# Kernel optimization log

Hardware: AMD Instinct MI355X
Metric: run time of the kernel (lower is better)

## Reference

```python
import jax, jax.numpy as jnp
import numpy as np


def setup_inputs() -> dict:
    key = jax.random.key(0)
    k1, k2, k3, k4 = jax.random.split(key, 4)
    B, C, H, W = 8, 256, 64, 64
    x = jax.random.normal(k1, (B, C, H, W), dtype=jnp.float32)
    wq = jax.random.normal(k2, (1, C), dtype=jnp.float32) * (1.0 / np.sqrt(C))
    wk = jax.random.normal(k3, (1, C), dtype=jnp.float32) * (1.0 / np.sqrt(C))
    wv = jax.random.normal(k4, (C, C), dtype=jnp.float32) * (1.0 / np.sqrt(C))
    gamma = jnp.zeros((1,), dtype=jnp.float32)
    return {"x": x, "wq": wq, "wk": wk, "wv": wv, "gamma": gamma}


def reference(x, wq, wk, wv, gamma):
    B, C, H, W = x.shape
    N = H * W
    xf = x.reshape(B, C, N)                      # [B, C, N]
    # 1x1 convs == channel matmuls
    f = jnp.einsum('oc,bcn->bon', wq, xf)        # [B, 1, N]
    g = jnp.einsum('oc,bcn->bon', wk, xf)        # [B, 1, N]
    h = jnp.einsum('oc,bcn->bon', wv, xf)        # [B, C, N]
    # scores[b, i, j] = f[b, 0, i] * g[b, 0, j]  -> [B, N, N]
    scores = jnp.einsum('bi,bj->bij', f[:, 0, :], g[:, 0, :])
    # softmax over dim=1 (rows), matching torch F.softmax(..., dim=1)
    beta = jax.nn.softmax(scores, axis=1)        # [B, N, N]
    gam = gamma[0]
    o = (1.0 - gam) * jnp.einsum('bcn,bnm->bcm', h, beta) + gam * xf
    return o.reshape(B, C, H, W)
```

## Files before the change

kernel.cpp:

```cpp
#include <hip/hip_runtime.h>
#include <math.h>

#define BQ 8
#define CQ 256
#define NQ 4096
#define MT 128
#define NSUP 64

typedef short s16x8 __attribute__((ext_vector_type(8)));
typedef short s16x4 __attribute__((ext_vector_type(4)));
typedef float f32x4 __attribute__((ext_vector_type(4)));
typedef unsigned int uint;

static __device__ __forceinline__ float4 ld4(const float* p) { return *(const float4*)p; }

static constexpr float LOG2E = 1.4426950408889634f;

static __device__ __forceinline__ short f2bf(float f) {
    return __builtin_bit_cast(short, (__bf16)f);
}
static __device__ __forceinline__ uint fkey(float f) {
    uint b = __builtin_bit_cast(uint, f);
    return b ^ (0x80000000u | (uint)((int)b >> 31));
}
static __device__ __forceinline__ float fdec(uint u) {
    uint b = (u & 0x80000000u) ? (u ^ 0x80000000u) : ~u;
    return __builtin_bit_cast(float, b);
}

__global__ void k_fg(const float* __restrict__ x, const float* __restrict__ wq,
                     const float* __restrict__ wk, float* __restrict__ fs,
                     float* __restrict__ g, short* __restrict__ xbf,
                     uint* __restrict__ fmxu, uint* __restrict__ fmnu) {
    int b = blockIdx.y;
    int t = threadIdx.x;
    int nl = (t & 31) * 2;
    int cg = t >> 5;
    int n = blockIdx.x * 64 + nl;
    const float* xb = x + (size_t)b * CQ * NQ + n;
    uint* xo = (uint*)(xbf + (size_t)b * CQ * NQ + n);
    float f0 = 0.f, f1 = 0.f, g0 = 0.f, g1 = 0.f;
    int c0 = cg * 32;
#pragma unroll 8
    for (int c = c0; c < c0 + 32; ++c) {
        float2 v = *(const float2*)&xb[(size_t)c * NQ];
        f0 = fmaf(wq[c], v.x, f0);
        f1 = fmaf(wq[c], v.y, f1);
        g0 = fmaf(wk[c], v.x, g0);
        g1 = fmaf(wk[c], v.y, g1);
        uint p = (uint)(unsigned short)f2bf(v.x) | ((uint)(unsigned short)f2bf(v.y) << 16);
        xo[c * (NQ / 2)] = p;
    }
    __shared__ float sf[8][64], sg2[8][64];
    sf[cg][nl] = f0;  sf[cg][nl + 1] = f1;
    sg2[cg][nl] = g0; sg2[cg][nl + 1] = g1;
    __syncthreads();
    if (t < 64) {
        float f = 0.f, gg = 0.f;
#pragma unroll
        for (int i = 0; i < 8; ++i) { f += sf[i][t]; gg += sg2[i][t]; }
        f *= LOG2E;
        fs[b * NQ + blockIdx.x * 64 + t] = f;
        g[b * NQ + blockIdx.x * 64 + t]  = gg;
        float mx = f, mn = f;
#pragma unroll
        for (int off = 32; off; off >>= 1) {
            mx = fmaxf(mx, __shfl_xor(mx, off));
            mn = fminf(mn, __shfl_xor(mn, off));
        }
        if (t == 0) {
            atomicMax(&fmxu[b], fkey(mx));
            atomicMin(&fmnu[b], fkey(mn));
        }
    }
}

#define FLDS_OFF 131072
#define ZBUF_OFF 147456
#define SMEM_BYTES 149504

#define STAGE_PAIR(bufp, pi)                                                       \
    {                                                                              \
        int cpair2_ = (pi) * 2;                                                    \
        _Pragma("unroll")                                                          \
        for (int r2_ = 0; r2_ < 4; ++r2_) {                                        \
            int off_ = tid * 16 + r2_ * 8192;                                      \
            int half_ = off_ >> 14;                                                \
            int rem_ = off_ & 16383;                                               \
            int row_ = rem_ >> 6;                                                  \
            int lq_ = ((rem_ >> 4) & 3) ^ ((row_ >> 1) & 3);                       \
            const short* src_ = xb + (size_t)row_ * NQ + (cpair2_ + half_) * 32 + lq_ * 8; \
            __builtin_amdgcn_global_load_lds(                                      \
                (const __attribute__((address_space(1))) void*)src_,               \
                (__attribute__((address_space(3))) void*)((bufp) + off_), 16, 0, 0); \
        }                                                                          \
    }

__global__ void __launch_bounds__(512, 1) k_attn(
    const short* __restrict__ xbf, const float* __restrict__ fsp,
    const float* __restrict__ gp, const uint* __restrict__ fmxu,
    const uint* __restrict__ fmnu, const float* __restrict__ wv,
    const float* __restrict__ x, const float* __restrict__ gamma,
    float* __restrict__ out) {
    __shared__ __align__(16) char smem[SMEM_BYTES];

    int bid = blockIdx.x;
    int b = bid & 7;
    int mblk = bid >> 3;
    int m0 = mblk * MT;
    int tid = threadIdx.x;
    int l = tid & 63;
    int w = tid >> 6;
    int ws = w & 1;
    int wm = (w >> 1) & 1;
    int wc = w >> 2;
    int q = l >> 4;
    int cr = l & 15;
    int qp16 = (q ^ ((cr >> 1) & 3)) * 16;

    const short* xb = xbf + (size_t)b * CQ * NQ;
    const float* fb = fsp + b * NQ;

#pragma unroll
    for (int r2 = 0; r2 < 2; ++r2) {
        int off = tid * 16 + r2 * 8192;
        __builtin_amdgcn_global_load_lds(
            (const __attribute__((address_space(1))) void*)(fb + (off >> 2)),
            (__attribute__((address_space(3))) void*)(smem + FLDS_OFF + off), 16, 0, 0);
    }
    STAGE_PAIR(smem, 0)

    float fmx = fdec(fmxu[b]), fmn = fdec(fmnu[b]);
    const float* gb = gp + b * NQ;
    float gj[4], nM[4], zac[4];
#pragma unroll
    for (int jm = 0; jm < 4; ++jm) {
        float gv = gb[m0 + wm * 64 + jm * 16 + cr];
        gj[jm] = gv;
        nM[jm] = -((gv >= 0.f) ? gv * fmx : gv * fmn);
        zac[jm] = 0.f;
    }

    f32x4 acc[8][4];
#pragma unroll
    for (int jc = 0; jc < 8; ++jc)
#pragma unroll
        for (int jm = 0; jm < 4; ++jm) acc[jc][jm] = (f32x4){0.f, 0.f, 0.f, 0.f};

    __syncthreads();

    for (int s = 0; s < NSUP; ++s) {
        char* nbuf = smem + ((s & 1) ^ 1) * 32768;
        if (s < NSUP - 1) STAGE_PAIR(nbuf, s + 1)

        int chunk = 2 * s + ws;
        const char* cbuf = smem + (s & 1) * 32768 + ws * 16384;
        const float* fls = (const float*)(smem + FLDS_OFF) + chunk * 32;
        float4 fqa = *(const float4*)(fls + q * 8);
        float4 fqb = *(const float4*)(fls + q * 8 + 4);
        float fq[8] = {fqa.x, fqa.y, fqa.z, fqa.w, fqb.x, fqb.y, fqb.z, fqb.w};
        s16x8 bv[4];
#pragma unroll
        for (int jm = 0; jm < 4; ++jm) {
            float z = zac[jm];
#pragma unroll
            for (int i = 0; i < 8; ++i) {
                float e = __builtin_amdgcn_exp2f(fmaf(fq[i], gj[jm], nM[jm]));
                z += e;
                bv[jm][i] = f2bf(e);
            }
            zac[jm] = z;
        }
#pragma unroll
        for (int jc = 0; jc < 8; ++jc) {
            s16x8 av = *(const s16x8*)(cbuf + (wc * 128 + jc * 16 + cr) * 64 + qp16);
#pragma unroll
            for (int jm = 0; jm < 4; ++jm)
                acc[jc][jm] = __builtin_amdgcn_mfma_f32_16x16x32_bf16(av, bv[jm], acc[jc][jm], 0, 0, 0);
        }
        __syncthreads();
    }

    float zf[4];
#pragma unroll
    for (int jm = 0; jm < 4; ++jm) {
        float z = zac[jm];
        z += __shfl_xor(z, 16);
        z += __shfl_xor(z, 32);
        zf[jm] = z;
    }
    float* zb = (float*)(smem + ZBUF_OFF);
    if (q == 0) {
#pragma unroll
        for (int jm = 0; jm < 4; ++jm) zb[w * 64 + jm * 16 + cr] = zf[jm];
    }
    __syncthreads();
#pragma unroll
    for (int jm = 0; jm < 4; ++jm) zf[jm] += zb[(w ^ 1) * 64 + jm * 16 + cr];

    {
        int p = wc * 2 + wm;
        float* mrg = (float*)(smem + p * 32768);
        if (ws == 1) {
#pragma unroll
            for (int jc = 0; jc < 8; ++jc)
#pragma unroll
                for (int jm = 0; jm < 4; ++jm)
                    *(f32x4*)(mrg + ((jc * 4 + jm) * 64 + l) * 4) = acc[jc][jm];
        }
        __syncthreads();
        if (ws == 0) {
#pragma unroll
            for (int jc = 0; jc < 8; ++jc)
#pragma unroll
                for (int jm = 0; jm < 4; ++jm) {
                    f32x4 o = *(const f32x4*)(mrg + ((jc * 4 + jm) * 64 + l) * 4);
                    acc[jc][jm] += o;
                }
        }
        __syncthreads();
    }

    if (ws == 0) {
        float rzl[4];
#pragma unroll
        for (int jm = 0; jm < 4; ++jm) rzl[jm] = 1.0f / zf[jm];
#pragma unroll
        for (int jc = 0; jc < 8; ++jc) {
#pragma unroll
            for (int jm = 0; jm < 4; ++jm) {
                int mloc = wm * 64 + jm * 16 + cr;
                int cb = (wc * 256 + jc * 32 + q * 8) ^ ((mloc & 7) << 4);
                s16x4 v;
#pragma unroll
                for (int r = 0; r < 4; ++r) v[r] = f2bf(acc[jc][jm][r] * rzl[jm]);
                *(s16x4*)(smem + mloc * 512 + cb) = v;
            }
        }
    }
    __syncthreads();

    int co0 = w * 32;
    f32x4 acc2[2][8];
#pragma unroll
    for (int j2 = 0; j2 < 2; ++j2)
#pragma unroll
        for (int jm2 = 0; jm2 < 8; ++jm2) acc2[j2][jm2] = (f32x4){0.f, 0.f, 0.f, 0.f};

#pragma unroll 2
    for (int ks = 0; ks < 8; ++ks) {
        s16x8 a2[2];
#pragma unroll
        for (int j2 = 0; j2 < 2; ++j2) {
            const float* wr = wv + (size_t)(co0 + j2 * 16 + cr) * CQ + ks * 32 + q * 8;
            float4 wa = ld4(wr);
            float4 wb = ld4(wr + 4);
            a2[j2][0] = f2bf(wa.x); a2[j2][1] = f2bf(wa.y);
            a2[j2][2] = f2bf(wa.z); a2[j2][3] = f2bf(wa.w);
            a2[j2][4] = f2bf(wb.x); a2[j2][5] = f2bf(wb.y);
            a2[j2][6] = f2bf(wb.z); a2[j2][7] = f2bf(wb.w);
        }
#pragma unroll
        for (int jm2 = 0; jm2 < 8; ++jm2) {
            int mloc = jm2 * 16 + cr;
            s16x8 b2 = *(const s16x8*)(smem + mloc * 512 + ((ks * 64 + q * 16) ^ ((mloc & 7) << 4)));
#pragma unroll
            for (int j2 = 0; j2 < 2; ++j2)
                acc2[j2][jm2] = __builtin_amdgcn_mfma_f32_16x16x32_bf16(a2[j2], b2, acc2[j2][jm2], 0, 0, 0);
        }
    }

    float gam = gamma[0];
    float omg = 1.f - gam;
    if (gam != 0.f) {
#pragma unroll
        for (int j2 = 0; j2 < 2; ++j2)
#pragma unroll
            for (int jm2 = 0; jm2 < 8; ++jm2)
#pragma unroll
                for (int r = 0; r < 4; ++r) {
                    int c_out = co0 + j2 * 16 + q * 4 + r;
                    size_t idx = ((size_t)b * CQ + c_out) * NQ + m0 + jm2 * 16 + cr;
                    __builtin_nontemporal_store(
                        fmaf(gam, x[idx], acc2[j2][jm2][r] * omg), out + idx);
                }
    } else {
#pragma unroll
        for (int j2 = 0; j2 < 2; ++j2)
#pragma unroll
            for (int jm2 = 0; jm2 < 8; ++jm2)
#pragma unroll
                for (int r = 0; r < 4; ++r) {
                    int c_out = co0 + j2 * 16 + q * 4 + r;
                    size_t idx = ((size_t)b * CQ + c_out) * NQ + m0 + jm2 * 16 + cr;
                    __builtin_nontemporal_store(acc2[j2][jm2][r] * omg, out + idx);
                }
    }
}

extern "C" void kernel_launch(void* const* d_in, const int* in_sizes, int n_in,
                              void* d_out, int out_size, void* d_ws, size_t ws_size,
                              hipStream_t stream) {
    const float* x     = (const float*)d_in[0];
    const float* wq    = (const float*)d_in[1];
    const float* wk    = (const float*)d_in[2];
    const float* wv    = (const float*)d_in[3];
    const float* gamma = (const float*)d_in[4];
    float* out = (float*)d_out;

    float* ws  = (float*)d_ws;
    float* fs  = ws;
    float* g   = ws + BQ * NQ;
    uint* fmxu = (uint*)(ws + 2 * BQ * NQ);
    uint* fmnu = fmxu + 8;
    short* xbf = (short*)(ws + 2 * BQ * NQ + 64);

    hipMemsetAsync(fmxu, 0x00, 32, stream);
    hipMemsetAsync(fmnu, 0xFF, 32, stream);
    hipLaunchKernelGGL(k_fg, dim3(NQ / 64, BQ), dim3(256), 0, stream,
                       x, wq, wk, fs, g, xbf, fmxu, fmnu);
    hipLaunchKernelGGL(k_attn, dim3(BQ * (NQ / MT)), dim3(512), 0, stream,
                       xbf, fs, g, fmxu, fmnu, wv, x, gamma, out);
}
```

Baseline: 119.8 us.

## Double attention block to 1024 threads, halving per-wave tiles and staging work

Doubles the attention kernel block from 512 to 1024 threads (16 waves). Each wave now owns 32 instead of 64 output columns in the score/value MFMA phase and 16 instead of 32 output channels in the projection phase, which halves accumulator registers and adds more waves for latency hiding. The staging macro is replaced by precomputed per-thread source/destination pointers, so each thread issues two LDS-direct loads per step. The trade-off is more waves sharing the same LDS buffers and barriers, repeated exp work per wave for the same columns, and the __launch_bounds__(1024,4) hint combined with ~146KB of LDS per block.

```diff
diff --git a/kernel.cpp b/kernel.cpp
--- a/kernel.cpp
+++ b/kernel.cpp
@@ -79,24 +79,7 @@
 #define ZBUF_OFF 147456
 #define SMEM_BYTES 149504
 
-#define STAGE_PAIR(bufp, pi)                                                       \
-    {                                                                              \
-        int cpair2_ = (pi) * 2;                                                    \
-        _Pragma("unroll")                                                          \
-        for (int r2_ = 0; r2_ < 4; ++r2_) {                                        \
-            int off_ = tid * 16 + r2_ * 8192;                                      \
-            int half_ = off_ >> 14;                                                \
-            int rem_ = off_ & 16383;                                               \
-            int row_ = rem_ >> 6;                                                  \
-            int lq_ = ((rem_ >> 4) & 3) ^ ((row_ >> 1) & 3);                       \
-            const short* src_ = xb + (size_t)row_ * NQ + (cpair2_ + half_) * 32 + lq_ * 8; \
-            __builtin_amdgcn_global_load_lds(                                      \
-                (const __attribute__((address_space(1))) void*)src_,               \
-                (__attribute__((address_space(3))) void*)((bufp) + off_), 16, 0, 0); \
-        }                                                                          \
-    }
-
-__global__ void __launch_bounds__(512, 1) k_attn(
+__global__ void __launch_bounds__(1024, 4) k_attn(
     const short* __restrict__ xbf, const float* __restrict__ fsp,
     const float* __restrict__ gp, const uint* __restrict__ fmxu,
     const uint* __restrict__ fmnu, const float* __restrict__ wv,
@@ -112,8 +95,8 @@
     int l = tid & 63;
     int w = tid >> 6;
     int ws = w & 1;
-    int wm = (w >> 1) & 1;
-    int wc = w >> 2;
+    int wm = (w >> 1) & 3;
+    int wc = w >> 3;
     int q = l >> 4;
     int cr = l & 15;
     int qp16 = (q ^ ((cr >> 1) & 3)) * 16;
@@ -121,47 +104,65 @@
     const short* xb = xbf + (size_t)b * CQ * NQ;
     const float* fb = fsp + b * NQ;
 
-#pragma unroll
-    for (int r2 = 0; r2 < 2; ++r2) {
-        int off = tid * 16 + r2 * 8192;
-        __builtin_amdgcn_global_load_lds(
-            (const __attribute__((address_space(1))) void*)(fb + (off >> 2)),
-            (__attribute__((address_space(3))) void*)(smem + FLDS_OFF + off), 16, 0, 0);
-    }
-    STAGE_PAIR(smem, 0)
+    int dst0 = tid * 16;
+    int dst1 = tid * 16 + 16384;
+    int srow = tid >> 2;
+    int slq = (tid & 3) ^ ((srow >> 1) & 3);
+    const short* src0 = xb + (size_t)srow * NQ + slq * 8;
+    const short* src1 = src0 + 32;
+
+    __builtin_amdgcn_global_load_lds(
+        (const __attribute__((address_space(1))) void*)(fb + tid * 4),
+        (__attribute__((address_space(3))) void*)(smem + FLDS_OFF + tid * 16), 16, 0, 0);
+    __builtin_amdgcn_global_load_lds(
+        (const __attribute__((address_space(1))) void*)src0,
+        (__attribute__((address_space(3))) void*)(smem + dst0), 16, 0, 0);
+    __builtin_amdgcn_global_load_lds(
+        (const __attribute__((address_space(1))) void*)src1,
+        (__attribute__((address_space(3))) void*)(smem + dst1), 16, 0, 0);
+    src0 += 64;
+    src1 += 64;
 
     float fmx = fdec(fmxu[b]), fmn = fdec(fmnu[b]);
     const float* gb = gp + b * NQ;
-    float gj[4], nM[4], zac[4];
-#pragma unroll
-    for (int jm = 0; jm < 4; ++jm) {
-        float gv = gb[m0 + wm * 64 + jm * 16 + cr];
+    float gj[2], nM[2], zac[2];
+#pragma unroll
+    for (int jm = 0; jm < 2; ++jm) {
+        float gv = gb[m0 + wm * 32 + jm * 16 + cr];
         gj[jm] = gv;
         nM[jm] = -((gv >= 0.f) ? gv * fmx : gv * fmn);
         zac[jm] = 0.f;
     }
 
-    f32x4 acc[8][4];
+    f32x4 acc[8][2];
 #pragma unroll
     for (int jc = 0; jc < 8; ++jc)
 #pragma unroll
-        for (int jm = 0; jm < 4; ++jm) acc[jc][jm] = (f32x4){0.f, 0.f, 0.f, 0.f};
+        for (int jm = 0; jm < 2; ++jm) acc[jc][jm] = (f32x4){0.f, 0.f, 0.f, 0.f};
 
     __syncthreads();
 
     for (int s = 0; s < NSUP; ++s) {
-        char* nbuf = smem + ((s & 1) ^ 1) * 32768;
-        if (s < NSUP - 1) STAGE_PAIR(nbuf, s + 1)
-
+        if (s < NSUP - 1) {
+            char* nbuf = smem + ((s + 1) & 1) * 32768;
+            __builtin_amdgcn_global_load_lds(
+                (const __attribute__((address_space(1))) void*)src0,
+                (__attribute__((address_space(3))) void*)(nbuf + dst0), 16, 0, 0);
+            __builtin_amdgcn_global_load_lds(
+                (const __attribute__((address_space(1))) void*)src1,
+                (__attribute__((address_space(3))) void*)(nbuf + dst1), 16, 0, 0);
+            src0 += 64;
+            src1 += 64;
+        }
         int chunk = 2 * s + ws;
         const char* cbuf = smem + (s & 1) * 32768 + ws * 16384;
         const float* fls = (const float*)(smem + FLDS_OFF) + chunk * 32;
         float4 fqa = *(const float4*)(fls + q * 8);
         float4 fqb = *(const float4*)(fls + q * 8 + 4);
         float fq[8] = {fqa.x, fqa.y, fqa.z, fqa.w, fqb.x, fqb.y, fqb.z, fqb.w};
-        s16x8 bv[4];
-#pragma unroll
-        for (int jm = 0; jm < 4; ++jm) {
+        s16x8 bv[2];
+#pragma unroll
+        for (int jm = 0; jm < 2; ++jm) {
             float z = zac[jm];
 #pragma unroll
             for (int i = 0; i < 8; ++i) {
@@ -174,16 +175,15 @@
 #pragma unroll
         for (int jc = 0; jc < 8; ++jc) {
             s16x8 av = *(const s16x8*)(cbuf + (wc * 128 + jc * 16 + cr) * 64 + qp16);
-#pragma unroll
-            for (int jm = 0; jm < 4; ++jm)
-                acc[jc][jm] = __builtin_amdgcn_mfma_f32_16x16x32_bf16(av, bv[jm], acc[jc][jm], 0, 0, 0);
+            acc[jc][0] = __builtin_amdgcn_mfma_f32_16x16x32_bf16(av, bv[0], acc[jc][0], 0, 0, 0);
+            acc[jc][1] = __builtin_amdgcn_mfma_f32_16x16x32_bf16(av, bv[1], acc[jc][1], 0, 0, 0);
         }
         __syncthreads();
     }
 
-    float zf[4];
-#pragma unroll
-    for (int jm = 0; jm < 4; ++jm) {
+    float zf[2];
+#pragma unroll
+    for (int jm = 0; jm < 2; ++jm) {
         float z = zac[jm];
         z += __shfl_xor(z, 16);
         z += __shfl_xor(z, 32);
@@ -192,29 +192,29 @@
     float* zb = (float*)(smem + ZBUF_OFF);
     if (q == 0) {
 #pragma unroll
-        for (int jm = 0; jm < 4; ++jm) zb[w * 64 + jm * 16 + cr] = zf[jm];
+        for (int jm = 0; jm < 2; ++jm) zb[w * 32 + jm * 16 + cr] = zf[jm];
     }
     __syncthreads();
 #pragma unroll
-    for (int jm = 0; jm < 4; ++jm) zf[jm] += zb[(w ^ 1) * 64 + jm * 16 + cr];
+    for (int jm = 0; jm < 2; ++jm) zf[jm] += zb[(w ^ 1) * 32 + jm * 16 + cr];
 
     {
-        int p = wc * 2 + wm;
-        float* mrg = (float*)(smem + p * 32768);
+        int p = wc * 4 + wm;
+        float* mrg = (float*)(smem + p * 16384);
         if (ws == 1) {
 #pragma unroll
             for (int jc = 0; jc < 8; ++jc)
 #pragma unroll
-                for (int jm = 0; jm < 4; ++jm)
-                    *(f32x4*)(mrg + ((jc * 4 + jm) * 64 + l) * 4) = acc[jc][jm];
+                for (int jm = 0; jm < 2; ++jm)
+                    *(f32x4*)(mrg + ((jc * 2 + jm) * 64 + l) * 4) = acc[jc][jm];
         }
         __syncthreads();
         if (ws == 0) {
 #pragma unroll
             for (int jc = 0; jc < 8; ++jc)
 #pragma unroll
-                for (int jm = 0; jm < 4; ++jm) {
-                    f32x4 o = *(const f32x4*)(mrg + ((jc * 4 + jm) * 64 + l) * 4);
+                for (int jm = 0; jm < 2; ++jm) {
+                    f32x4 o = *(const f32x4*)(mrg + ((jc * 2 + jm) * 64 + l) * 4);
                     acc[jc][jm] += o;
                 }
         }
@@ -222,14 +222,14 @@
     }
 
     if (ws == 0) {
-        float rzl[4];
-#pragma unroll
-        for (int jm = 0; jm < 4; ++jm) rzl[jm] = 1.0f / zf[jm];
+        float rzl[2];
+#pragma unroll
+        for (int jm = 0; jm < 2; ++jm) rzl[jm] = 1.0f / zf[jm];
 #pragma unroll
         for (int jc = 0; jc < 8; ++jc) {
 #pragma unroll
-            for (int jm = 0; jm < 4; ++jm) {
-                int mloc = wm * 64 + jm * 16 + cr;
+            for (int jm = 0; jm < 2; ++jm) {
+                int mloc = wm * 32 + jm * 16 + cr;
                 int cb = (wc * 256 + jc * 32 + q * 8) ^ ((mloc & 7) << 4);
                 s16x4 v;
 #pragma unroll
@@ -240,33 +240,28 @@
     }
     __syncthreads();
 
-    int co0 = w * 32;
-    f32x4 acc2[2][8];
-#pragma unroll
-    for (int j2 = 0; j2 < 2; ++j2)
-#pragma unroll
-        for (int jm2 = 0; jm2 < 8; ++jm2) acc2[j2][jm2] = (f32x4){0.f, 0.f, 0.f, 0.f};
+    int co0 = w * 16;
+    f32x4 acc2[8];
+#pragma unroll
+    for (int jm2 = 0; jm2 < 8; ++jm2) acc2[jm2] = (f32x4){0.f, 0.f, 0.f, 0.f};
 
 #pragma unroll 2
     for (int ks = 0; ks < 8; ++ks) {
-        s16x8 a2[2];
-#pragma unroll
-        for (int j2 = 0; j2 < 2; ++j2) {
-            const float* wr = wv + (size_t)(co0 + j2 * 16 + cr) * CQ + ks * 32 + q * 8;
+        s16x8 a2;
+        {
+            const float* wr = wv + (size_t)(co0 + cr) * CQ + ks * 32 + q * 8;
             float4 wa = ld4(wr);
             float4 wb = ld4(wr + 4);
-            a2[j2][0] = f2bf(wa.x); a2[j2][1] = f2bf(wa.y);
-            a2[j2][2] = f2bf(wa.z); a2[j2][3] = f2bf(wa.w);
-            a2[j2][4] = f2bf(wb.x); a2[j2][5] = f2bf(wb.y);
-            a2[j2][6] = f2bf(wb.z); a2[j2][7] = f2bf(wb.w);
+            a2[0] = f2bf(wa.x); a2[1] = f2bf(wa.y);
+            a2[2] = f2bf(wa.z); a2[3] = f2bf(wa.w);
+            a2[4] = f2bf(wb.x); a2[5] = f2bf(wb.y);
+            a2[6] = f2bf(wb.z); a2[7] = f2bf(wb.w);
         }
 #pragma unroll
         for (int jm2 = 0; jm2 < 8; ++jm2) {
             int mloc = jm2 * 16 + cr;
             s16x8 b2 = *(const s16x8*)(smem + mloc * 512 + ((ks * 64 + q * 16) ^ ((mloc & 7) << 4)));
-#pragma unroll
-            for (int j2 = 0; j2 < 2; ++j2)
-                acc2[j2][jm2] = __builtin_amdgcn_mfma_f32_16x16x32_bf16(a2[j2], b2, acc2[j2][jm2], 0, 0, 0);
+            acc2[jm2] = __builtin_amdgcn_mfma_f32_16x16x32_bf16(a2, b2, acc2[jm2], 0, 0, 0);
         }
     }
 
@@ -274,27 +269,23 @@
     float omg = 1.f - gam;
     if (gam != 0.f) {
 #pragma unroll
-        for (int j2 = 0; j2 < 2; ++j2)
-#pragma unroll
-            for (int jm2 = 0; jm2 < 8; ++jm2)
-#pragma unroll
-                for (int r = 0; r < 4; ++r) {
-                    int c_out = co0 + j2 * 16 + q * 4 + r;
-                    size_t idx = ((size_t)b * CQ + c_out) * NQ + m0 + jm2 * 16 + cr;
-                    __builtin_nontemporal_store(
-                        fmaf(gam, x[idx], acc2[j2][jm2][r] * omg), out + idx);
-                }
+        for (int jm2 = 0; jm2 < 8; ++jm2)
+#pragma unroll
+            for (int r = 0; r < 4; ++r) {
+                int c_out = co0 + q * 4 + r;
+                size_t idx = ((size_t)b * CQ + c_out) * NQ + m0 + jm2 * 16 + cr;
+                __builtin_nontemporal_store(
+                    fmaf(gam, x[idx], acc2[jm2][r] * omg), out + idx);
+            }
     } else {
 #pragma unroll
-        for (int j2 = 0; j2 < 2; ++j2)
-#pragma unroll
-            for (int jm2 = 0; jm2 < 8; ++jm2)
-#pragma unroll
-                for (int r = 0; r < 4; ++r) {
-                    int c_out = co0 + j2 * 16 + q * 4 + r;
-                    size_t idx = ((size_t)b * CQ + c_out) * NQ + m0 + jm2 * 16 + cr;
-                    __builtin_nontemporal_store(acc2[j2][jm2][r] * omg, out + idx);
-                }
+        for (int jm2 = 0; jm2 < 8; ++jm2)
+#pragma unroll
+            for (int r = 0; r < 4; ++r) {
+                int c_out = co0 + q * 4 + r;
+                size_t idx = ((size_t)b * CQ + c_out) * NQ + m0 + jm2 * 16 + cr;
+                __builtin_nontemporal_store(acc2[jm2][r] * omg, out + idx);
+            }
     }
 }
 
@@ -319,6 +310,6 @@
     hipMemsetAsync(fmnu, 0xFF, 32, stream);
     hipLaunchKernelGGL(k_fg, dim3(NQ / 64, BQ), dim3(256), 0, stream,
                        x, wq, wk, fs, g, xbf, fmxu, fmnu);
-    hipLaunchKernelGGL(k_attn, dim3(BQ * (NQ / MT)), dim3(512), 0, stream,
+    hipLaunchKernelGGL(k_attn, dim3(BQ * (NQ / MT)), dim3(1024), 0, stream,
                        xbf, fs, g, fmxu, fmnu, wv, x, gamma, out);
 }
```

After: 117.3 us. -2.1%, faster.

## Halve m-tile to 64, raise occupancy, compute softmax denominators via MFMA

Applied to the files above, without the earlier changes.

Shrinks the per-block output column tile from 128 to 64, halving the accumulator registers and shared memory so launch bounds can allow four blocks per CU instead of one. It also drops the LDS staging of f, reading it straight from global memory, precomputes the load addresses once, and accumulates the softmax row sums with an MFMA against a vector of ones instead of scalar adds and shuffles. The cost is that twice as many blocks each re-stream the full bf16 x for their batch, doubling global/L2 traffic for the x operand and the exp work per column.

```diff
diff --git a/kernel.cpp b/kernel.cpp
--- a/kernel.cpp
+++ b/kernel.cpp
@@ -4,7 +4,7 @@
 #define BQ 8
 #define CQ 256
 #define NQ 4096
-#define MT 128
+#define MT 64
 #define NSUP 64
 
 typedef short s16x8 __attribute__((ext_vector_type(8)));
@@ -75,28 +75,10 @@
     }
 }
 
-#define FLDS_OFF 131072
-#define ZBUF_OFF 147456
-#define SMEM_BYTES 149504
-
-#define STAGE_PAIR(bufp, pi)                                                       \
-    {                                                                              \
-        int cpair2_ = (pi) * 2;                                                    \
-        _Pragma("unroll")                                                          \
-        for (int r2_ = 0; r2_ < 4; ++r2_) {                                        \
-            int off_ = tid * 16 + r2_ * 8192;                                      \
-            int half_ = off_ >> 14;                                                \
-            int rem_ = off_ & 16383;                                               \
-            int row_ = rem_ >> 6;                                                  \
-            int lq_ = ((rem_ >> 4) & 3) ^ ((row_ >> 1) & 3);                       \
-            const short* src_ = xb + (size_t)row_ * NQ + (cpair2_ + half_) * 32 + lq_ * 8; \
-            __builtin_amdgcn_global_load_lds(                                      \
-                (const __attribute__((address_space(1))) void*)src_,               \
-                (__attribute__((address_space(3))) void*)((bufp) + off_), 16, 0, 0); \
-        }                                                                          \
-    }
-
-__global__ void __launch_bounds__(512, 1) k_attn(
+#define ZBUF_OFF 65536
+#define SMEM_BYTES 66560
+
+__global__ void __launch_bounds__(512, 4) k_attn(
     const short* __restrict__ xbf, const float* __restrict__ fsp,
     const float* __restrict__ gp, const uint* __restrict__ fmxu,
     const uint* __restrict__ fmnu, const float* __restrict__ wv,
@@ -121,100 +103,110 @@
     const short* xb = xbf + (size_t)b * CQ * NQ;
     const float* fb = fsp + b * NQ;
 
-#pragma unroll
-    for (int r2 = 0; r2 < 2; ++r2) {
-        int off = tid * 16 + r2 * 8192;
+    const short* srcs[4];
+    int dsts[4];
+#pragma unroll
+    for (int r2 = 0; r2 < 4; ++r2) {
+        int row = (tid >> 2) + (r2 & 1) * 128;
+        int half = r2 >> 1;
+        int lq = (tid & 3) ^ ((row >> 1) & 3);
+        srcs[r2] = xb + (size_t)row * NQ + half * 32 + lq * 8;
+        dsts[r2] = tid * 16 + r2 * 8192;
+    }
+
+#pragma unroll
+    for (int r2 = 0; r2 < 4; ++r2) {
         __builtin_amdgcn_global_load_lds(
-            (const __attribute__((address_space(1))) void*)(fb + (off >> 2)),
-            (__attribute__((address_space(3))) void*)(smem + FLDS_OFF + off), 16, 0, 0);
-    }
-    STAGE_PAIR(smem, 0)
+            (const __attribute__((address_space(1))) void*)srcs[r2],
+            (__attribute__((address_space(3))) void*)(smem + dsts[r2]), 16, 0, 0);
+        srcs[r2] += 64;
+    }
 
     float fmx = fdec(fmxu[b]), fmn = fdec(fmnu[b]);
     const float* gb = gp + b * NQ;
-    float gj[4], nM[4], zac[4];
-#pragma unroll
-    for (int jm = 0; jm < 4; ++jm) {
-        float gv = gb[m0 + wm * 64 + jm * 16 + cr];
+    float gj[2], nM[2];
+#pragma unroll
+    for (int jm = 0; jm < 2; ++jm) {
+        float gv = gb[m0 + wm * 32 + jm * 16 + cr];
         gj[jm] = gv;
         nM[jm] = -((gv >= 0.f) ? gv * fmx : gv * fmn);
-        zac[jm] = 0.f;
-    }
-
-    f32x4 acc[8][4];
+    }
+
+    s16x8 ones;
+#pragma unroll
+    for (int i = 0; i < 8; ++i) ones[i] = (short)0x3F80;
+
+    f32x4 acc[8][2];
 #pragma unroll
     for (int jc = 0; jc < 8; ++jc)
 #pragma unroll
-        for (int jm = 0; jm < 4; ++jm) acc[jc][jm] = (f32x4){0.f, 0.f, 0.f, 0.f};
+        for (int jm = 0; jm < 2; ++jm) acc[jc][jm] = (f32x4){0.f, 0.f, 0.f, 0.f};
+    f32x4 accz[2] = {(f32x4){0.f, 0.f, 0.f, 0.f}, (f32x4){0.f, 0.f, 0.f, 0.f}};
 
     __syncthreads();
 
     for (int s = 0; s < NSUP; ++s) {
-        char* nbuf = smem + ((s & 1) ^ 1) * 32768;
-        if (s < NSUP - 1) STAGE_PAIR(nbuf, s + 1)
-
+        if (s < NSUP - 1) {
+            char* nbuf = smem + ((s + 1) & 1) * 32768;
+#pragma unroll
+            for (int r2 = 0; r2 < 4; ++r2) {
+                __builtin_amdgcn_global_load_lds(
+                    (const __attribute__((address_space(1))) void*)srcs[r2],
+                    (__attribute__((address_space(3))) void*)(nbuf + dsts[r2]), 16, 0, 0);
+                srcs[r2] += 64;
+            }
+        }
         int chunk = 2 * s + ws;
         const char* cbuf = smem + (s & 1) * 32768 + ws * 16384;
-        const float* fls = (const float*)(smem + FLDS_OFF) + chunk * 32;
-        float4 fqa = *(const float4*)(fls + q * 8);
-        float4 fqb = *(const float4*)(fls + q * 8 + 4);
+        const float* fls = fb + chunk * 32;
+        float4 fqa = ld4(fls + q * 8);
+        float4 fqb = ld4(fls + q * 8 + 4);
         float fq[8] = {fqa.x, fqa.y, fqa.z, fqa.w, fqb.x, fqb.y, fqb.z, fqb.w};
-        s16x8 bv[4];
-#pragma unroll
-        for (int jm = 0; jm < 4; ++jm) {
-            float z = zac[jm];
-#pragma unroll
-            for (int i = 0; i < 8; ++i) {
-                float e = __builtin_amdgcn_exp2f(fmaf(fq[i], gj[jm], nM[jm]));
-                z += e;
-                bv[jm][i] = f2bf(e);
-            }
-            zac[jm] = z;
-        }
+        s16x8 bv[2];
+#pragma unroll
+        for (int jm = 0; jm < 2; ++jm) {
+#pragma unroll
+            for (int i = 0; i < 8; ++i)
+                bv[jm][i] = f2bf(__builtin_amdgcn_exp2f(fmaf(fq[i], gj[jm], nM[jm])));
+        }
+        accz[0] = __builtin_amdgcn_mfma_f32_16x16x32_bf16(ones, bv[0], accz[0], 0, 0, 0);
+        accz[1] = __builtin_amdgcn_mfma_f32_16x16x32_bf16(ones, bv[1], accz[1], 0, 0, 0);
 #pragma unroll
         for (int jc = 0; jc < 8; ++jc) {
             s16x8 av = *(const s16x8*)(cbuf + (wc * 128 + jc * 16 + cr) * 64 + qp16);
-#pragma unroll
-            for (int jm = 0; jm < 4; ++jm)
-                acc[jc][jm] = __builtin_amdgcn_mfma_f32_16x16x32_bf16(av, bv[jm], acc[jc][jm], 0, 0, 0);
+            acc[jc][0] = __builtin_amdgcn_mfma_f32_16x16x32_bf16(av, bv[0], acc[jc][0], 0, 0, 0);
+            acc[jc][1] = __builtin_amdgcn_mfma_f32_16x16x32_bf16(av, bv[1], acc[jc][1], 0, 0, 0);
         }
         __syncthreads();
     }
 
-    float zf[4];
-#pragma unroll
-    for (int jm = 0; jm < 4; ++jm) {
-        float z = zac[jm];
-        z += __shfl_xor(z, 16);
-        z += __shfl_xor(z, 32);
-        zf[jm] = z;
-    }
+    float zf[2] = {accz[0][0], accz[1][0]};
     float* zb = (float*)(smem + ZBUF_OFF);
     if (q == 0) {
 #pragma unroll
-        for (int jm = 0; jm < 4; ++jm) zb[w * 64 + jm * 16 + cr] = zf[jm];
+        for (int jm = 0; jm < 2; ++jm) zb[w * 32 + jm * 16 + cr] = zf[jm];
     }
     __syncthreads();
 #pragma unroll
-    for (int jm = 0; jm < 4; ++jm) zf[jm] += zb[(w ^ 1) * 64 + jm * 16 + cr];
+    for (int jm = 0; jm < 2; ++jm) zf[jm] += zb[(w ^ 1) * 32 + jm * 16 + cr];
 
     {
         int p = wc * 2 + wm;
-        float* mrg = (float*)(smem + p * 32768);
+        float* mrg = (float*)(smem + p * 16384);
         if (ws == 1) {
 #pragma unroll
             for (int jc = 0; jc < 8; ++jc)
 #pragma unroll
-                for (int jm = 0; jm < 4; ++jm)
-                    *(f32x4*)(mrg + ((jc * 4 + jm) * 64 + l) * 4) = acc[jc][jm];
+                for (int jm = 0; jm < 2; ++jm)
+                    *(f32x4*)(mrg + ((jc * 2 + jm) * 64 + l) * 4) = acc[jc][jm];
         }
         __syncthreads();
         if (ws == 0) {
 #pragma unroll
             for (int jc = 0; jc < 8; ++jc)
 #pragma unroll
-                for (int jm = 0; jm < 4; ++jm) {
-                    f32x4 o = *(const f32x4*)(mrg + ((jc * 4 + jm) * 64 + l) * 4);
+                for (int jm = 0; jm < 2; ++jm) {
+                    f32x4 o = *(const f32x4*)(mrg + ((jc * 2 + jm) * 64 + l) * 4);
                     acc[jc][jm] += o;
                 }
         }
@@ -222,14 +214,14 @@
     }
 
     if (ws == 0) {
-        float rzl[4];
-#pragma unroll
-        for (int jm = 0; jm < 4; ++jm) rzl[jm] = 1.0f / zf[jm];
+        float rzl[2];
+#pragma unroll
+        for (int jm = 0; jm < 2; ++jm) rzl[jm] = 1.0f / zf[jm];
 #pragma unroll
         for (int jc = 0; jc < 8; ++jc) {
 #pragma unroll
-            for (int jm = 0; jm < 4; ++jm) {
-                int mloc = wm * 64 + jm * 16 + cr;
+            for (int jm = 0; jm < 2; ++jm) {
+                int mloc = wm * 32 + jm * 16 + cr;
                 int cb = (wc * 256 + jc * 32 + q * 8) ^ ((mloc & 7) << 4);
                 s16x4 v;
 #pragma unroll
@@ -241,11 +233,11 @@
     __syncthreads();
 
     int co0 = w * 32;
-    f32x4 acc2[2][8];
+    f32x4 acc2[2][4];
 #pragma unroll
     for (int j2 = 0; j2 < 2; ++j2)
 #pragma unroll
-        for (int jm2 = 0; jm2 < 8; ++jm2) acc2[j2][jm2] = (f32x4){0.f, 0.f, 0.f, 0.f};
+        for (int jm2 = 0; jm2 < 4; ++jm2) acc2[j2][jm2] = (f32x4){0.f, 0.f, 0.f, 0.f};
 
 #pragma unroll 2
     for (int ks = 0; ks < 8; ++ks) {
@@ -261,7 +253,7 @@
             a2[j2][6] = f2bf(wb.z); a2[j2][7] = f2bf(wb.w);
         }
 #pragma unroll
-        for (int jm2 = 0; jm2 < 8; ++jm2) {
+        for (int jm2 = 0; jm2 < 4; ++jm2) {
             int mloc = jm2 * 16 + cr;
             s16x8 b2 = *(const s16x8*)(smem + mloc * 512 + ((ks * 64 + q * 16) ^ ((mloc & 7) << 4)));
 #pragma unroll
@@ -276,7 +268,7 @@
 #pragma unroll
         for (int j2 = 0; j2 < 2; ++j2)
 #pragma unroll
-            for (int jm2 = 0; jm2 < 8; ++jm2)
+            for (int jm2 = 0; jm2 < 4; ++jm2)
 #pragma unroll
                 for (int r = 0; r < 4; ++r) {
                     int c_out = co0 + j2 * 16 + q * 4 + r;
@@ -288,7 +280,7 @@
 #pragma unroll
         for (int j2 = 0; j2 < 2; ++j2)
 #pragma unroll
-            for (int jm2 = 0; jm2 < 8; ++jm2)
+            for (int jm2 = 0; jm2 < 4; ++jm2)
 #pragma unroll
                 for (int r = 0; r < 4; ++r) {
                     int c_out = co0 + j2 * 16 + q * 4 + r;
```

Result: slower. 129.2 us (+7.9%).

## Switch attention core to 32x32 MFMA with triple-buffered async LDS staging

Applied to the files above, without the earlier changes.

Replaces the 16x16x32 bf16 MFMA tiles with 32x32x16 tiles and moves from a double-buffered staging loop to a three-slot ring with explicit vmcnt waits and raw barriers. The f values are prefetched into registers one iteration ahead. LDS use shrinks so the launch bound can request two blocks per CU. The aim is to cut synchronisation stalls and LDS read traffic per MFMA, and to overlap global-to-LDS loads with the exp/MFMA work. The cost is higher register pressure from the 16-wide accumulators, and the hand-tuned waitcnt ordering could race if the counts are wrong.

```diff
diff --git a/kernel.cpp b/kernel.cpp
--- a/kernel.cpp
+++ b/kernel.cpp
@@ -10,6 +10,7 @@
 typedef short s16x8 __attribute__((ext_vector_type(8)));
 typedef short s16x4 __attribute__((ext_vector_type(4)));
 typedef float f32x4 __attribute__((ext_vector_type(4)));
+typedef float f32x16 __attribute__((ext_vector_type(16)));
 typedef unsigned int uint;
 
 static __device__ __forceinline__ float4 ld4(const float* p) { return *(const float4*)p; }
@@ -75,28 +76,14 @@
     }
 }
 
-#define FLDS_OFF 131072
-#define ZBUF_OFF 147456
-#define SMEM_BYTES 149504
-
-#define STAGE_PAIR(bufp, pi)                                                       \
-    {                                                                              \
-        int cpair2_ = (pi) * 2;                                                    \
-        _Pragma("unroll")                                                          \
-        for (int r2_ = 0; r2_ < 4; ++r2_) {                                        \
-            int off_ = tid * 16 + r2_ * 8192;                                      \
-            int half_ = off_ >> 14;                                                \
-            int rem_ = off_ & 16383;                                               \
-            int row_ = rem_ >> 6;                                                  \
-            int lq_ = ((rem_ >> 4) & 3) ^ ((row_ >> 1) & 3);                       \
-            const short* src_ = xb + (size_t)row_ * NQ + (cpair2_ + half_) * 32 + lq_ * 8; \
-            __builtin_amdgcn_global_load_lds(                                      \
-                (const __attribute__((address_space(1))) void*)src_,               \
-                (__attribute__((address_space(3))) void*)((bufp) + off_), 16, 0, 0); \
-        }                                                                          \
-    }
-
-__global__ void __launch_bounds__(512, 1) k_attn(
+#define FLDS_OFF 98304
+#define ZBUF_OFF 131072
+#define SMEM_BYTES 133120
+
+#define GSRC(p) (const __attribute__((address_space(1))) void*)(p)
+#define LDST(p) (__attribute__((address_space(3))) void*)(p)
+
+__global__ void __launch_bounds__(512, 2) k_attn(
     const short* __restrict__ xbf, const float* __restrict__ fsp,
     const float* __restrict__ gp, const uint* __restrict__ fmxu,
     const uint* __restrict__ fmnu, const float* __restrict__ wv,
@@ -114,129 +101,192 @@
     int ws = w & 1;
     int wm = (w >> 1) & 1;
     int wc = w >> 2;
+    int col = l & 31;
+    int hi = l >> 5;
     int q = l >> 4;
     int cr = l & 15;
-    int qp16 = (q ^ ((cr >> 1) & 3)) * 16;
 
     const short* xb = xbf + (size_t)b * CQ * NQ;
     const float* fb = fsp + b * NQ;
 
-#pragma unroll
-    for (int r2 = 0; r2 < 2; ++r2) {
-        int off = tid * 16 + r2 * 8192;
-        __builtin_amdgcn_global_load_lds(
-            (const __attribute__((address_space(1))) void*)(fb + (off >> 2)),
-            (__attribute__((address_space(3))) void*)(smem + FLDS_OFF + off), 16, 0, 0);
-    }
-    STAGE_PAIR(smem, 0)
+    int dst = tid * 16;
+    int srow0 = tid >> 2;
+    int srow1 = srow0 + 128;
+    const short* src0 = xb + (size_t)srow0 * NQ + ((tid & 3) ^ ((srow0 >> 1) & 3)) * 8;
+    const short* src1 = xb + (size_t)srow1 * NQ + ((tid & 3) ^ ((srow1 >> 1) & 3)) * 8;
+
+    __builtin_amdgcn_global_load_lds(GSRC(fb + tid * 4),
+        LDST(smem + FLDS_OFF + dst), 16, 0, 0);
+    __builtin_amdgcn_global_load_lds(GSRC(fb + tid * 4 + 2048),
+        LDST(smem + FLDS_OFF + 8192 + dst), 16, 0, 0);
+#pragma unroll
+    for (int k = 0; k < 4; ++k) {
+        __builtin_amdgcn_global_load_lds(GSRC(src0 + k * 32),
+            LDST(smem + k * 16384 + dst), 16, 0, 0);
+        __builtin_amdgcn_global_load_lds(GSRC(src1 + k * 32),
+            LDST(smem + k * 16384 + 8192 + dst), 16, 0, 0);
+    }
 
     float fmx = fdec(fmxu[b]), fmn = fdec(fmnu[b]);
     const float* gb = gp + b * NQ;
-    float gj[4], nM[4], zac[4];
-#pragma unroll
-    for (int jm = 0; jm < 4; ++jm) {
-        float gv = gb[m0 + wm * 64 + jm * 16 + cr];
-        gj[jm] = gv;
-        nM[jm] = -((gv >= 0.f) ? gv * fmx : gv * fmn);
-        zac[jm] = 0.f;
-    }
-
-    f32x4 acc[8][4];
-#pragma unroll
-    for (int jc = 0; jc < 8; ++jc)
-#pragma unroll
-        for (int jm = 0; jm < 4; ++jm) acc[jc][jm] = (f32x4){0.f, 0.f, 0.f, 0.f};
-
+    float gj[2], nM[2], zac[2] = {0.f, 0.f};
+#pragma unroll
+    for (int mt = 0; mt < 2; ++mt) {
+        float gv = gb[m0 + wm * 64 + mt * 32 + col];
+        gj[mt] = gv;
+        nM[mt] = -((gv >= 0.f) ? gv * fmx : gv * fmn);
+    }
+
+    int rowoff[4], rkey[4];
+#pragma unroll
+    for (int ct = 0; ct < 4; ++ct) {
+        int row = wc * 128 + ct * 32 + col;
+        rowoff[ct] = row * 64;
+        rkey[ct] = ((row >> 1) & 3) * 16;
+    }
+
+    f32x16 acc[4][2];
+#pragma unroll
+    for (int ct = 0; ct < 4; ++ct)
+#pragma unroll
+        for (int mt = 0; mt < 2; ++mt)
+#pragma unroll
+            for (int r = 0; r < 16; ++r) acc[ct][mt][r] = 0.f;
+
+    asm volatile("s_waitcnt vmcnt(8)" ::: "memory");
+    __builtin_amdgcn_s_barrier();
+    const float* fl0 = (const float*)(smem + FLDS_OFF);
+    float4 fc[4];
+    {
+        int n0 = ws * 32;
+        fc[0] = *(const float4*)(fl0 + n0 + 8 * hi);
+        fc[1] = *(const float4*)(fl0 + n0 + 8 * hi + 4);
+        fc[2] = *(const float4*)(fl0 + n0 + 16 + 8 * hi);
+        fc[3] = *(const float4*)(fl0 + n0 + 16 + 8 * hi + 4);
+    }
+
+    int rs = 0;
+    int ssl = 4;
+    for (int p = 0; p < NSUP; ++p) {
+        asm volatile("s_waitcnt vmcnt(4)" ::: "memory");
+        __builtin_amdgcn_s_barrier();
+        {
+            int chA = (2 * p + 4) & 127;
+            __builtin_amdgcn_global_load_lds(GSRC(src0 + chA * 32),
+                LDST(smem + ssl * 16384 + dst), 16, 0, 0);
+            __builtin_amdgcn_global_load_lds(GSRC(src1 + chA * 32),
+                LDST(smem + ssl * 16384 + 8192 + dst), 16, 0, 0);
+            __builtin_amdgcn_global_load_lds(GSRC(src0 + chA * 32 + 32),
+                LDST(smem + (ssl + 1) * 16384 + dst), 16, 0, 0);
+            __builtin_amdgcn_global_load_lds(GSRC(src1 + chA * 32 + 32),
+                LDST(smem + (ssl + 1) * 16384 + 8192 + dst), 16, 0, 0);
+        }
+        s16x8 bv[2][2];
+#pragma unroll
+        for (int kt = 0; kt < 2; ++kt) {
+            float fq[8] = {fc[kt*2].x, fc[kt*2].y, fc[kt*2].z, fc[kt*2].w,
+                           fc[kt*2+1].x, fc[kt*2+1].y, fc[kt*2+1].z, fc[kt*2+1].w};
+#pragma unroll
+            for (int mt = 0; mt < 2; ++mt) {
+                float z = zac[mt];
+#pragma unroll
+                for (int i = 0; i < 8; ++i) {
+                    float e = __builtin_amdgcn_exp2f(fmaf(fq[i], gj[mt], nM[mt]));
+                    z += e;
+                    bv[mt][kt][i] = f2bf(e);
+                }
+                zac[mt] = z;
+            }
+        }
+        {
+            int nn = ((2 * p + 2 + ws) & 127) * 32;
+            fc[0] = *(const float4*)(fl0 + nn + 8 * hi);
+            fc[1] = *(const float4*)(fl0 + nn + 8 * hi + 4);
+            fc[2] = *(const float4*)(fl0 + nn + 16 + 8 * hi);
+            fc[3] = *(const float4*)(fl0 + nn + 16 + 8 * hi + 4);
+        }
+        const char* cbuf = smem + (rs + ws) * 16384;
+#pragma unroll
+        for (int kt = 0; kt < 2; ++kt) {
+            int lslot = (kt * 2 + hi) * 16;
+#pragma unroll
+            for (int ct = 0; ct < 4; ++ct) {
+                s16x8 av = *(const s16x8*)(cbuf + rowoff[ct] + (lslot ^ rkey[ct]));
+                acc[ct][0] = __builtin_amdgcn_mfma_f32_32x32x16_bf16(av, bv[0][kt], acc[ct][0], 0, 0, 0);
+                acc[ct][1] = __builtin_amdgcn_mfma_f32_32x32x16_bf16(av, bv[1][kt], acc[ct][1], 0, 0, 0);
+            }
+        }
+        rs += 2;  if (rs >= 6) rs -= 6;
+        ssl += 2; if (ssl >= 6) ssl -= 6;
+    }
     __syncthreads();
 
-    for (int s = 0; s < NSUP; ++s) {
-        char* nbuf = smem + ((s & 1) ^ 1) * 32768;
-        if (s < NSUP - 1) STAGE_PAIR(nbuf, s + 1)
-
-        int chunk = 2 * s + ws;
-        const char* cbuf = smem + (s & 1) * 32768 + ws * 16384;
-        const float* fls = (const float*)(smem + FLDS_OFF) + chunk * 32;
-        float4 fqa = *(const float4*)(fls + q * 8);
-        float4 fqb = *(const float4*)(fls + q * 8 + 4);
-        float fq[8] = {fqa.x, fqa.y, fqa.z, fqa.w, fqb.x, fqb.y, fqb.z, fqb.w};
-        s16x8 bv[4];
-#pragma unroll
-        for (int jm = 0; jm < 4; ++jm) {
-            float z = zac[jm];
-#pragma unroll
-            for (int i = 0; i < 8; ++i) {
-                float e = __builtin_amdgcn_exp2f(fmaf(fq[i], gj[jm], nM[jm]));
-                z += e;
-                bv[jm][i] = f2bf(e);
-            }
-            zac[jm] = z;
-        }
-#pragma unroll
-        for (int jc = 0; jc < 8; ++jc) {
-            s16x8 av = *(const s16x8*)(cbuf + (wc * 128 + jc * 16 + cr) * 64 + qp16);
-#pragma unroll
-            for (int jm = 0; jm < 4; ++jm)
-                acc[jc][jm] = __builtin_amdgcn_mfma_f32_16x16x32_bf16(av, bv[jm], acc[jc][jm], 0, 0, 0);
-        }
-        __syncthreads();
-    }
-
-    float zf[4];
-#pragma unroll
-    for (int jm = 0; jm < 4; ++jm) {
-        float z = zac[jm];
-        z += __shfl_xor(z, 16);
+    float zf[2];
+#pragma unroll
+    for (int mt = 0; mt < 2; ++mt) {
+        float z = zac[mt];
         z += __shfl_xor(z, 32);
-        zf[jm] = z;
-    }
-    float* zb = (float*)(smem + ZBUF_OFF);
-    if (q == 0) {
-#pragma unroll
-        for (int jm = 0; jm < 4; ++jm) zb[w * 64 + jm * 16 + cr] = zf[jm];
-    }
-    __syncthreads();
-#pragma unroll
-    for (int jm = 0; jm < 4; ++jm) zf[jm] += zb[(w ^ 1) * 64 + jm * 16 + cr];
-
+        zf[mt] = z;
+    }
     {
-        int p = wc * 2 + wm;
-        float* mrg = (float*)(smem + p * 32768);
+        float* zb = (float*)(smem + ZBUF_OFF);
+        if (l < 32) {
+#pragma unroll
+            for (int mt = 0; mt < 2; ++mt) zb[w * 64 + mt * 32 + l] = zf[mt];
+        }
+        int p8 = wc * 2 + wm;
+        float* mrg = (float*)(smem + p8 * 32768);
         if (ws == 1) {
 #pragma unroll
-            for (int jc = 0; jc < 8; ++jc)
-#pragma unroll
-                for (int jm = 0; jm < 4; ++jm)
-                    *(f32x4*)(mrg + ((jc * 4 + jm) * 64 + l) * 4) = acc[jc][jm];
+            for (int ct = 0; ct < 4; ++ct)
+#pragma unroll
+                for (int mt = 0; mt < 2; ++mt) {
+                    int fi = ct * 2 + mt;
+#pragma unroll
+                    for (int j = 0; j < 4; ++j) {
+                        f32x4 v = {acc[ct][mt][4*j], acc[ct][mt][4*j+1],
+                                   acc[ct][mt][4*j+2], acc[ct][mt][4*j+3]};
+                        *(f32x4*)(mrg + ((fi * 4 + j) * 64 + l) * 4) = v;
+                    }
+                }
         }
         __syncthreads();
         if (ws == 0) {
 #pragma unroll
-            for (int jc = 0; jc < 8; ++jc)
-#pragma unroll
-                for (int jm = 0; jm < 4; ++jm) {
-                    f32x4 o = *(const f32x4*)(mrg + ((jc * 4 + jm) * 64 + l) * 4);
-                    acc[jc][jm] += o;
-                }
-        }
+            for (int ct = 0; ct < 4; ++ct)
+#pragma unroll
+                for (int mt = 0; mt < 2; ++mt) {
+                    int fi = ct * 2 + mt;
+#pragma unroll
+                    for (int j = 0; j < 4; ++j) {
+                        f32x4 o = *(const f32x4*)(mrg + ((fi * 4 + j) * 64 + l) * 4);
+#pragma unroll
+                        for (int i = 0; i < 4; ++i) acc[ct][mt][4*j+i] += o[i];
+                    }
+                }
+        }
+#pragma unroll
+        for (int mt = 0; mt < 2; ++mt) zf[mt] += zb[(w ^ 1) * 64 + mt * 32 + col];
         __syncthreads();
     }
 
     if (ws == 0) {
-        float rzl[4];
-#pragma unroll
-        for (int jm = 0; jm < 4; ++jm) rzl[jm] = 1.0f / zf[jm];
-#pragma unroll
-        for (int jc = 0; jc < 8; ++jc) {
-#pragma unroll
-            for (int jm = 0; jm < 4; ++jm) {
-                int mloc = wm * 64 + jm * 16 + cr;
-                int cb = (wc * 256 + jc * 32 + q * 8) ^ ((mloc & 7) << 4);
-                s16x4 v;
-#pragma unroll
-                for (int r = 0; r < 4; ++r) v[r] = f2bf(acc[jc][jm][r] * rzl[jm]);
-                *(s16x4*)(smem + mloc * 512 + cb) = v;
+        float rzl[2] = {1.0f / zf[0], 1.0f / zf[1]};
+#pragma unroll
+        for (int ct = 0; ct < 4; ++ct)
+#pragma unroll
+            for (int mt = 0; mt < 2; ++mt) {
+                int mloc = wm * 64 + mt * 32 + col;
+                int key = (mloc & 7) << 4;
+#pragma unroll
+                for (int j = 0; j < 4; ++j) {
+                    int cb = (wc * 256 + ct * 64 + 16 * j + 8 * hi) ^ key;
+                    s16x4 v;
+#pragma unroll
+                    for (int i = 0; i < 4; ++i) v[i] = f2bf(acc[ct][mt][4*j+i] * rzl[mt]);
+                    *(s16x4*)(smem + mloc * 512 + cb) = v;
+                }
             }
-        }
     }
     __syncthreads();
 
```

After: 121.9 us. Within noise of the previous version (+1.8%).
